# Optimization experiments

Measured on AMD Instinct MI355X. Metric: run time of the kernel, lower is better.

The kernel has to match this reference:

```python
import jax, jax.numpy as jnp
import numpy as np

B, T, C, H = 4, 4096, 1024, 128

def setup_inputs() -> dict:
    key = jax.random.key(0)
    kx, kk, kq, kv = jax.random.split(key, 4)
    scale = 1.0 / np.sqrt(C)  # mimic Linear init scale
    return {
        'x':  jax.random.normal(kx, (B, T, C), dtype=jnp.float32),
        'Wk': jax.random.normal(kk, (C, H), dtype=jnp.float32) * scale,
        'Wq': jax.random.normal(kq, (C, H), dtype=jnp.float32) * scale,
        'Wv': jax.random.normal(kv, (C, H), dtype=jnp.float32) * scale,
    }

def reference(x, Wk, Wq, Wv):
    # x: [B,T,C]; projections to [B,T,H]
    k = jnp.einsum('btc,ch->bth', x, Wk)
    q = jnp.einsum('btc,ch->bth', x, Wq)
    v = jnp.einsum('btc,ch->bth', x, Wv)
    scale = jnp.asarray(x.shape[-1] and (k.shape[-1] ** -0.5), dtype=x.dtype)
    # scores: [B,T,T]
    scores = jnp.einsum('bqh,bkh->bqk', q, k) * scale
    Tn = x.shape[1]
    causal = jnp.tril(jnp.ones((Tn, Tn), dtype=bool))
    scores = jnp.where(causal[None, :, :], scores, -jnp.inf)
    attn = jax.nn.softmax(scores, axis=-1)
    # dropout=0.0 -> identity
    out = jnp.einsum('bqk,bkh->bqh', attn, v)
    return out
```

## Files before the change

### kernel.cpp

```cpp
#include <hip/hip_runtime.h>
#include <hip/hip_bf16.h>
#include <math.h>

#define B_ 4
#define T_ 4096
#define C_ 1024
#define H_ 128
#define SCALE 0.08838834764831845f

typedef __attribute__((ext_vector_type(8))) short bf16x8;
typedef __attribute__((ext_vector_type(4))) float f32x4;

__device__ __forceinline__ unsigned short f2bf(float f) {
    union { float f; unsigned u; } x; x.f = f;
    unsigned r = x.u + 0x7FFF + ((x.u >> 16) & 1);
    return (unsigned short)(r >> 16);
}
__device__ __forceinline__ float bf2f(unsigned short u) {
    union { unsigned u; float f; } x; x.u = ((unsigned)u) << 16;
    return x.f;
}
__device__ __forceinline__ unsigned cvt_pk_bf16(float a, float b) {
    unsigned r;
    asm("v_cvt_pk_bf16_f32 %0, %1, %2" : "=v"(r) : "v"(a), "v"(b));
    return r;
}

#define GLOAD16(gsrc, ldst)                                                        \
    __builtin_amdgcn_global_load_lds(                                              \
        (const __attribute__((address_space(1))) unsigned int*)(gsrc),             \
        (__attribute__((address_space(3))) unsigned int*)(ldst), 16, 0, 0)

__global__ __launch_bounds__(256) void wtrans_kernel(
        const float* __restrict__ Wk, const float* __restrict__ Wq,
        const float* __restrict__ Wv, unsigned short* __restrict__ Wt) {
    int tid = blockIdx.x * 256 + threadIdx.x;
    int t = tid >> 17;
    int r = tid & 131071;
    int c = r >> 7;
    int h = r & 127;
    const float* W = (t == 0) ? Wk : (t == 1) ? Wq : Wv;
    Wt[t * 131072 + h * 1024 + c] = f2bf(W[r]);
}

__global__ __launch_bounds__(256) void qkv_gemm(
        const float* __restrict__ x, const unsigned short* __restrict__ Wt,
        unsigned short* __restrict__ qkv) {
    __shared__ unsigned short As[64][72];
    __shared__ unsigned short Bs[384][72];

    const int m0 = blockIdx.x * 64;
    const int tid = threadIdx.x;
    const int lane = tid & 63;
    const int w = tid >> 6;
    const int fr = lane & 15;
    const int fq = lane >> 4;

    f32x4 acc[6][4];
#pragma unroll
    for (int i = 0; i < 6; i++)
#pragma unroll
        for (int rf = 0; rf < 4; rf++) acc[i][rf] = f32x4{0.f, 0.f, 0.f, 0.f};

    for (int k0 = 0; k0 < C_; k0 += 64) {
        __syncthreads();
        {
            int row = tid >> 2;
            int coff = (tid & 3) * 16;
            const float* src = x + (long)(m0 + row) * C_ + k0 + coff;
            unsigned short tmp[16];
#pragma unroll
            for (int i = 0; i < 4; i++) {
                float4 v = ((const float4*)src)[i];
                tmp[i*4+0] = f2bf(v.x); tmp[i*4+1] = f2bf(v.y);
                tmp[i*4+2] = f2bf(v.z); tmp[i*4+3] = f2bf(v.w);
            }
            uint4* dst = (uint4*)&As[row][coff];
            dst[0] = ((uint4*)tmp)[0];
            dst[1] = ((uint4*)tmp)[1];
        }
#pragma unroll
        for (int i = 0; i < 12; i++) {
            int idx = tid + i * 256;
            int row = idx >> 3;
            int coff = (idx & 7) * 8;
            *(uint4*)&Bs[row][coff] =
                *(const uint4*)(Wt + (long)row * 1024 + k0 + coff);
        }
        __syncthreads();

#pragma unroll
        for (int kk = 0; kk < 2; kk++) {
            bf16x8 a[4], bb[6];
#pragma unroll
            for (int rf = 0; rf < 4; rf++)
                a[rf] = *(const bf16x8*)&As[rf*16 + fr][kk*32 + fq*8];
#pragma unroll
            for (int i = 0; i < 6; i++)
                bb[i] = *(const bf16x8*)&Bs[(w*6 + i)*16 + fr][kk*32 + fq*8];
#pragma unroll
            for (int i = 0; i < 6; i++)
#pragma unroll
                for (int rf = 0; rf < 4; rf++)
                    acc[i][rf] = __builtin_amdgcn_mfma_f32_16x16x32_bf16(
                        a[rf], bb[i], acc[i][rf], 0, 0, 0);
        }
    }
#pragma unroll
    for (int i = 0; i < 6; i++) {
        int nf = w*6 + i;
        int t = nf >> 3;
        int col = (nf & 7) * 16 + fr;
#pragma unroll
        for (int rf = 0; rf < 4; rf++)
#pragma unroll
            for (int r = 0; r < 4; r++) {
                int row = m0 + rf*16 + fq*4 + r;
                qkv[(long)t * (16384L * 128) + (long)row * 128 + col] = f2bf(acc[i][rf][r]);
            }
    }
}

__global__ __launch_bounds__(256) void vtrans_kernel(
        const unsigned short* __restrict__ v, unsigned short* __restrict__ vT) {
    __shared__ unsigned short tile[64][136];
    const int t0 = (blockIdx.x & 63) * 64;
    const int b = blockIdx.x >> 6;
    const int tid = threadIdx.x;
#pragma unroll
    for (int i = 0; i < 4; i++) {
        int idx = tid + i * 256;
        int tr = idx >> 4, coff = (idx & 15) * 8;
        *(uint4*)&tile[tr][coff] =
            *(const uint4*)(v + ((long)(b * T_ + t0 + tr)) * H_ + coff);
    }
    __syncthreads();
#pragma unroll
    for (int i = 0; i < 4; i++) {
        int idx = tid + i * 256;
        int h = idx >> 3, ts = (idx & 7) * 8;
        unsigned short tmp[8];
#pragma unroll
        for (int j = 0; j < 8; j++) tmp[j] = tile[ts + j][h];
        *(uint4*)(vT + ((long)(b * H_ + h)) * T_ + t0 + ts) = *(uint4*)tmp;
    }
}

__global__ __launch_bounds__(512, 4) void flash6_kernel(
        const unsigned short* __restrict__ qkv,
        const unsigned short* __restrict__ vT,
        unsigned short* __restrict__ po0, unsigned short* __restrict__ po1,
        unsigned short* __restrict__ po2, unsigned short* __restrict__ po3,
        float* __restrict__ pm, float* __restrict__ pl) {
    __shared__ unsigned short k_lds[2][64][128];
    __shared__ unsigned short v_lds[2][128][64];

    const int n = blockIdx.x;
    const int half = n >> 8;
    const int m = n & 255;
    const int b = (m & 7) >> 1;
    const int r = ((m >> 3) << 1) | (m & 1);
    const int jj = r & 31;
    const int pq = r >> 5;
    const int qt = half ? (31 - jj) : jj;
    const int p = half * 2 + pq;
    const int q0 = qt * 128;
    const int ntt = (qt + 1) * 2;
    const int t0 = (p * ntt) >> 2;
    const int t1 = ((p + 1) * ntt) >> 2;

    const int tid = threadIdx.x;
    const int w = tid >> 6;
    const int lane = tid & 63;
    const int fr = lane & 15;
    const int fq = lane >> 4;

    const unsigned short* kbase = qkv + (long)b * T_ * H_;
    const unsigned short* vbase = vT + (long)b * H_ * T_;

    const int kcolb0 = ((lane & 15) << 4) ^ ((((lane >> 4)) & 7) << 4);
    const int kcolb1 = ((lane & 15) << 4) ^ (((4 + (lane >> 4)) & 7) << 4);
    const int krl = lane >> 4;
    const int vrl = lane >> 3;
    const int vcolb = ((lane & 7) << 4) ^ (vrl << 4);
    unsigned short* const klds_flat = &k_lds[0][0][0];
    unsigned short* const vlds_flat = &v_lds[0][0][0];

    const int scol = ((fq ^ (fr & 7)) << 4);

    bf16x8 qf[4];
    {
        const unsigned short* qptr = qkv + 2097152 + ((long)b*T_ + q0 + w*16 + fr) * H_;
#pragma unroll
        for (int ks = 0; ks < 4; ks++)
            qf[ks] = *(const bf16x8*)(qptr + ks*32 + fq*8);
    }

    f32x4 acc[8];
#pragma unroll
    for (int i = 0; i < 8; i++) acc[i] = f32x4{0.f, 0.f, 0.f, 0.f};
    float m_r = -INFINITY, l_r = 0.f;
    const int qrow = q0 + w*16 + fr;

    int cur = 0;
    if (t0 < t1) {
        const int kv0 = t0 * 64;
#pragma unroll
        for (int i = 0; i < 2; i++) {
            int kcolb = i ? kcolb1 : kcolb0;
            GLOAD16(kbase + (long)(kv0 + 8*w + 4*i + krl) * 128 + (kcolb >> 1),
                    klds_flat + w*1024 + i*512);
            GLOAD16(vbase + (long)(16*w + 8*i + vrl) * 4096 + kv0 + (vcolb >> 1),
                    vlds_flat + w*1024 + i*512);
        }
    }

    for (int t = t0; t < t1; ++t) {
        const int kv0 = t * 64;
        __syncthreads();
        if (t + 1 < t1) {
            const int kv0n = kv0 + 64;
            const int boff = (cur ^ 1) * 8192;
#pragma unroll
            for (int i = 0; i < 2; i++) {
                int kcolb = i ? kcolb1 : kcolb0;
                GLOAD16(kbase + (long)(kv0n + 8*w + 4*i + krl) * 128 + (kcolb >> 1),
                        klds_flat + boff + w*1024 + i*512);
                GLOAD16(vbase + (long)(16*w + 8*i + vrl) * 4096 + kv0n + (vcolb >> 1),
                        vlds_flat + boff + w*1024 + i*512);
            }
            asm volatile("s_waitcnt vmcnt(4)" ::: "memory");
        } else {
            asm volatile("s_waitcnt vmcnt(0)" ::: "memory");
        }
        __syncthreads();

        const char* kl = (const char*)k_lds + cur*16384 + fr*256;
        const char* vl = (const char*)v_lds + cur*16384 + fr*128;

        f32x4 s[4];
#pragma unroll
        for (int sf = 0; sf < 4; sf++) s[sf] = f32x4{0.f,0.f,0.f,0.f};
        __builtin_amdgcn_s_setprio(1);
#pragma unroll
        for (int sf = 0; sf < 4; sf++)
#pragma unroll
            for (int ks = 0; ks < 4; ks++) {
                bf16x8 kf = *(const bf16x8*)(kl + sf*4096 + (scol ^ (ks << 6)));
                s[sf] = __builtin_amdgcn_mfma_f32_16x16x32_bf16(kf, qf[ks], s[sf], 0, 0, 0);
            }
        __builtin_amdgcn_s_setprio(0);

        float mx = -INFINITY;
        if (kv0 + 63 > q0 + 16*w) {
#pragma unroll
            for (int sf = 0; sf < 4; sf++)
#pragma unroll
                for (int rr = 0; rr < 4; rr++) {
                    int kv = kv0 + sf*16 + fq*4 + rr;
                    float sv = s[sf][rr] * SCALE;
                    sv = (kv > qrow) ? -INFINITY : sv;
                    s[sf][rr] = sv;
                    mx = fmaxf(mx, sv);
                }
        } else {
#pragma unroll
            for (int sf = 0; sf < 4; sf++)
#pragma unroll
                for (int rr = 0; rr < 4; rr++) {
                    float sv = s[sf][rr] * SCALE;
                    s[sf][rr] = sv;
                    mx = fmaxf(mx, sv);
                }
        }
        mx = fmaxf(mx, __shfl_xor(mx, 16, 64));
        mx = fmaxf(mx, __shfl_xor(mx, 32, 64));

        const bool skip = __all((m_r > -1e37f) & (mx - m_r <= 8.f));
        float msub;
        if (skip) {
            msub = m_r;
        } else {
            float mn = fmaxf(m_r, mx);
            msub = (mn == -INFINITY) ? 0.f : mn;
            float alpha = __expf(m_r - msub);
            m_r = mn;
#pragma unroll
            for (int hf = 0; hf < 8; hf++)
#pragma unroll
                for (int rr = 0; rr < 4; rr++) acc[hf][rr] *= alpha;
            l_r *= alpha;
        }

        float pv[4][4];
        float sum = 0.f;
#pragma unroll
        for (int sf = 0; sf < 4; sf++)
#pragma unroll
            for (int rr = 0; rr < 4; rr++) {
                float e = __expf(s[sf][rr] - msub);
                pv[sf][rr] = e;
                sum += e;
            }
        sum += __shfl_xor(sum, 16, 64);
        sum += __shfl_xor(sum, 32, 64);
        l_r += sum;

        unsigned pw[8];
#pragma unroll
        for (int sf = 0; sf < 4; sf++) {
            pw[2*sf]   = cvt_pk_bf16(pv[sf][0], pv[sf][1]);
            pw[2*sf+1] = cvt_pk_bf16(pv[sf][2], pv[sf][3]);
        }
        unsigned pbu[2][4];
        pbu[0][0]=0;pbu[0][1]=0;pbu[0][2]=0;pbu[0][3]=0;
        pbu[1][0]=0;pbu[1][1]=0;pbu[1][2]=0;pbu[1][3]=0;
        const int L1 = fr + 16 * ((fq & 1) * 2);
        const int L2 = L1 + 16;
        const int sel = (fq >> 1) & 1;
#pragma unroll
        for (int sf = 0; sf < 4; sf++) {
            unsigned w0 = (unsigned)__shfl((int)pw[2*sf],   L1, 64);
            unsigned w1 = (unsigned)__shfl((int)pw[2*sf+1], L1, 64);
            unsigned w2 = (unsigned)__shfl((int)pw[2*sf],   L2, 64);
            unsigned w3 = (unsigned)__shfl((int)pw[2*sf+1], L2, 64);
            if ((sf & 1) == sel) {
                int k2 = sf >> 1;
                pbu[k2][0] = w0; pbu[k2][1] = w1; pbu[k2][2] = w2; pbu[k2][3] = w3;
            }
        }
        union { unsigned u[4]; bf16x8 v; } pb0c, pb1c;
#pragma unroll
        for (int i = 0; i < 4; i++) { pb0c.u[i] = pbu[0][i]; pb1c.u[i] = pbu[1][i]; }
        bf16x8 pb0 = pb0c.v, pb1 = pb1c.v;

        __builtin_amdgcn_s_setprio(1);
#pragma unroll
        for (int hf = 0; hf < 8; hf++) {
            bf16x8 vf0 = *(const bf16x8*)(vl + hf*2048 + scol);
            bf16x8 vf1 = *(const bf16x8*)(vl + hf*2048 + (scol ^ 64));
            acc[hf] = __builtin_amdgcn_mfma_f32_16x16x32_bf16(vf0, pb0, acc[hf], 0, 0, 0);
            acc[hf] = __builtin_amdgcn_mfma_f32_16x16x32_bf16(vf1, pb1, acc[hf], 0, 0, 0);
        }
        __builtin_amdgcn_s_setprio(0);
        cur ^= 1;
    }

    unsigned short* po = (p == 0) ? po0 : (p == 1) ? po1 : (p == 2) ? po2 : po3;
    float linv = (l_r > 0.f) ? (1.0f / l_r) : 0.f;
    const long obase = ((long)b * T_ + qrow) * H_;
#pragma unroll
    for (int hf = 0; hf < 8; hf++) {
        unsigned u0 = cvt_pk_bf16(acc[hf][0] * linv, acc[hf][1] * linv);
        unsigned u1 = cvt_pk_bf16(acc[hf][2] * linv, acc[hf][3] * linv);
        uint2 uu; uu.x = u0; uu.y = u1;
        *(uint2*)(po + obase + hf*16 + fq*4) = uu;
    }
    if (fq == 0) {
        pm[p * 16384 + b * T_ + qrow] = m_r;
        pl[p * 16384 + b * T_ + qrow] = l_r;
    }
}

__global__ __launch_bounds__(256) void combine_kernel(
        const unsigned short* __restrict__ po0,
        const unsigned short* __restrict__ po1,
        const unsigned short* __restrict__ po2,
        const unsigned short* __restrict__ po3,
        const float* __restrict__ pm, const float* __restrict__ pl,
        float* __restrict__ out) {
    int idx = blockIdx.x * 256 + threadIdx.x;
    int row = idx >> 4;
    int seg = idx & 15;
    float mv[4], lv[4];
#pragma unroll
    for (int i = 0; i < 4; i++) { mv[i] = pm[i*16384 + row]; lv[i] = pl[i*16384 + row]; }
    float m = fmaxf(fmaxf(mv[0], mv[1]), fmaxf(mv[2], mv[3]));
    float wv[4]; float tot = 0.f;
#pragma unroll
    for (int i = 0; i < 4; i++) {
        wv[i] = (lv[i] > 0.f) ? __expf(mv[i] - m) * lv[i] : 0.f;
        tot += wv[i];
    }
    float inv = 1.0f / tot;
    long off = (long)row * H_ + seg * 8;
    unsigned short ua[8], ub[8], uc[8], ud[8];
    *(uint4*)ua = *(const uint4*)(po0 + off);
    *(uint4*)ub = *(const uint4*)(po1 + off);
    *(uint4*)uc = *(const uint4*)(po2 + off);
    *(uint4*)ud = *(const uint4*)(po3 + off);
    float* o = out + off;
#pragma unroll
    for (int j2 = 0; j2 < 8; j2++)
        o[j2] = inv * (wv[0] * bf2f(ua[j2]) + wv[1] * bf2f(ub[j2]) +
                       wv[2] * bf2f(uc[j2]) + wv[3] * bf2f(ud[j2]));
}

extern "C" void kernel_launch(void* const* d_in, const int* in_sizes, int n_in,
                              void* d_out, int out_size, void* d_ws, size_t ws_size,
                              hipStream_t stream) {
    (void)in_sizes; (void)n_in; (void)out_size; (void)ws_size;
    const float* x  = (const float*)d_in[0];
    const float* Wk = (const float*)d_in[1];
    const float* Wq = (const float*)d_in[2];
    const float* Wv = (const float*)d_in[3];
    float* out = (float*)d_out;

    unsigned short* Wt  = (unsigned short*)d_ws;
    unsigned short* qkv = Wt + 393216;
    unsigned short* vT  = qkv + 6291456;
    unsigned short* po0 = vT + 2097152;
    unsigned short* po1 = po0 + 2097152;
    unsigned short* po3 = po1 + 2097152;
    unsigned short* po2 = qkv + 4194304;
    float* pm = (float*)d_ws;
    float* pl = pm + 65536;

    wtrans_kernel<<<1536, 256, 0, stream>>>(Wk, Wq, Wv, Wt);
    qkv_gemm<<<256, 256, 0, stream>>>(x, Wt, qkv);
    vtrans_kernel<<<256, 256, 0, stream>>>(qkv + 4194304, vT);
    flash6_kernel<<<512, 512, 0, stream>>>(qkv, vT, po0, po1, po2, po3, pm, pl);
    combine_kernel<<<1024, 256, 0, stream>>>(po0, po1, po2, po3, pm, pl, out);
}
```

Before: 96.51 us.

## Double-buffer QKV GEMM, split N across blocks, fuse V transpose into epilogue

The QKV projection GEMM now splits the 384 output columns into two halves, so twice as many blocks run with fewer accumulators each. It double-buffers the x and W tiles, using global_load_lds async copies with swizzled LDS for W and register prefetch for x, and remaps block order for locality. The V output is written directly in transposed layout from the GEMM epilogue, which removes the separate vtrans kernel launch and its round trip through memory. In exchange, each x tile is loaded and converted twice, once per column half, and the transposed V writes are narrower and strided.

```diff
diff --git a/kernel.cpp b/kernel.cpp
--- a/kernel.cpp
+++ b/kernel.cpp
@@ -24,6 +24,14 @@
     unsigned r;
     asm("v_cvt_pk_bf16_f32 %0, %1, %2" : "=v"(r) : "v"(a), "v"(b));
     return r;
+}
+__device__ __forceinline__ void cvt16(const float4& a, const float4& b,
+                                      const float4& c, const float4& d,
+                                      unsigned short* t) {
+    t[0]=f2bf(a.x);  t[1]=f2bf(a.y);  t[2]=f2bf(a.z);  t[3]=f2bf(a.w);
+    t[4]=f2bf(b.x);  t[5]=f2bf(b.y);  t[6]=f2bf(b.z);  t[7]=f2bf(b.w);
+    t[8]=f2bf(c.x);  t[9]=f2bf(c.y);  t[10]=f2bf(c.z); t[11]=f2bf(c.w);
+    t[12]=f2bf(d.x); t[13]=f2bf(d.y); t[14]=f2bf(d.z); t[15]=f2bf(d.w);
 }
 
 #define GLOAD16(gsrc, ldst)                                                        \
@@ -43,106 +51,124 @@
     Wt[t * 131072 + h * 1024 + c] = f2bf(W[r]);
 }
 
-__global__ __launch_bounds__(256) void qkv_gemm(
+__global__ __launch_bounds__(256, 2) void qkv_gemm2(
         const float* __restrict__ x, const unsigned short* __restrict__ Wt,
-        unsigned short* __restrict__ qkv) {
-    __shared__ unsigned short As[64][72];
-    __shared__ unsigned short Bs[384][72];
-
-    const int m0 = blockIdx.x * 64;
+        unsigned short* __restrict__ qkv, unsigned short* __restrict__ vT) {
+    __shared__ unsigned short As[2][64][72];
+    __shared__ unsigned short Bs[2][192][64];
+
+    const int nsw = blockIdx.x;
+    const int sw = (nsw & 7) * 64 + (nsw >> 3);
+    const int m0 = (sw >> 1) * 64;
+    const int nh = sw & 1;
+
     const int tid = threadIdx.x;
     const int lane = tid & 63;
     const int w = tid >> 6;
     const int fr = lane & 15;
     const int fq = lane >> 4;
 
-    f32x4 acc[6][4];
+    const int xrow = tid >> 2, xco = (tid & 3) * 16;
+    const float* xsrc = x + (long)(m0 + xrow) * C_ + xco;
+    const int brl = lane >> 3;
+    const int bcolb = (((lane & 7) ^ brl) << 4);
+    unsigned short* const bs_flat = &Bs[0][0][0];
+    const unsigned short* wbase = Wt + (long)(nh * 192) * 1024;
+
+    f32x4 acc[3][4];
+#pragma unroll
+    for (int i = 0; i < 3; i++)
+#pragma unroll
+        for (int rf = 0; rf < 4; rf++) acc[i][rf] = f32x4{0.f, 0.f, 0.f, 0.f};
+
+    float4 xr0, xr1, xr2, xr3;
+    xr0 = ((const float4*)xsrc)[0]; xr1 = ((const float4*)xsrc)[1];
+    xr2 = ((const float4*)xsrc)[2]; xr3 = ((const float4*)xsrc)[3];
 #pragma unroll
     for (int i = 0; i < 6; i++)
-#pragma unroll
-        for (int rf = 0; rf < 4; rf++) acc[i][rf] = f32x4{0.f, 0.f, 0.f, 0.f};
-
-    for (int k0 = 0; k0 < C_; k0 += 64) {
+        GLOAD16(wbase + (long)(48*w + 8*i + brl) * 1024 + (bcolb >> 1),
+                bs_flat + (w*6 + i) * 512);
+    {
+        unsigned short tmp[16];
+        cvt16(xr0, xr1, xr2, xr3, tmp);
+        *(uint4*)&As[0][xrow][xco]     = ((uint4*)tmp)[0];
+        *(uint4*)&As[0][xrow][xco + 8] = ((uint4*)tmp)[1];
+    }
+
+    int cur = 0;
+    for (int k = 0; k < 16; ++k) {
         __syncthreads();
-        {
-            int row = tid >> 2;
-            int coff = (tid & 3) * 16;
-            const float* src = x + (long)(m0 + row) * C_ + k0 + coff;
-            unsigned short tmp[16];
-#pragma unroll
-            for (int i = 0; i < 4; i++) {
-                float4 v = ((const float4*)src)[i];
-                tmp[i*4+0] = f2bf(v.x); tmp[i*4+1] = f2bf(v.y);
-                tmp[i*4+2] = f2bf(v.z); tmp[i*4+3] = f2bf(v.w);
-            }
-            uint4* dst = (uint4*)&As[row][coff];
-            dst[0] = ((uint4*)tmp)[0];
-            dst[1] = ((uint4*)tmp)[1];
-        }
-#pragma unroll
-        for (int i = 0; i < 12; i++) {
-            int idx = tid + i * 256;
-            int row = idx >> 3;
-            int coff = (idx & 7) * 8;
-            *(uint4*)&Bs[row][coff] =
-                *(const uint4*)(Wt + (long)row * 1024 + k0 + coff);
+        const bool more = (k + 1) < 16;
+        if (more) {
+            const float* xs = xsrc + (k + 1) * 64;
+            xr0 = ((const float4*)xs)[0]; xr1 = ((const float4*)xs)[1];
+            xr2 = ((const float4*)xs)[2]; xr3 = ((const float4*)xs)[3];
+            const int boff = (cur ^ 1) * 12288;
+#pragma unroll
+            for (int i = 0; i < 6; i++)
+                GLOAD16(wbase + (long)(48*w + 8*i + brl) * 1024 + (k + 1) * 64 + (bcolb >> 1),
+                        bs_flat + boff + (w*6 + i) * 512);
+            asm volatile("s_waitcnt vmcnt(10)" ::: "memory");
+        } else {
+            asm volatile("s_waitcnt vmcnt(0)" ::: "memory");
         }
         __syncthreads();
 
+        const char* bsb = (const char*)bs_flat + cur * 24576;
+        __builtin_amdgcn_s_setprio(1);
 #pragma unroll
         for (int kk = 0; kk < 2; kk++) {
-            bf16x8 a[4], bb[6];
+            bf16x8 a[4], bb[3];
 #pragma unroll
             for (int rf = 0; rf < 4; rf++)
-                a[rf] = *(const bf16x8*)&As[rf*16 + fr][kk*32 + fq*8];
-#pragma unroll
-            for (int i = 0; i < 6; i++)
-                bb[i] = *(const bf16x8*)&Bs[(w*6 + i)*16 + fr][kk*32 + fq*8];
-#pragma unroll
-            for (int i = 0; i < 6; i++)
+                a[rf] = *(const bf16x8*)&As[cur][rf*16 + fr][kk*32 + fq*8];
+#pragma unroll
+            for (int i = 0; i < 3; i++) {
+                int row = (w*3 + i) * 16 + fr;
+                bb[i] = *(const bf16x8*)(bsb + row*128 + ((((kk<<2) + fq) ^ (fr & 7)) << 4));
+            }
+#pragma unroll
+            for (int i = 0; i < 3; i++)
 #pragma unroll
                 for (int rf = 0; rf < 4; rf++)
                     acc[i][rf] = __builtin_amdgcn_mfma_f32_16x16x32_bf16(
                         a[rf], bb[i], acc[i][rf], 0, 0, 0);
         }
-    }
-#pragma unroll
-    for (int i = 0; i < 6; i++) {
-        int nf = w*6 + i;
-        int t = nf >> 3;
-        int col = (nf & 7) * 16 + fr;
-#pragma unroll
-        for (int rf = 0; rf < 4; rf++)
-#pragma unroll
-            for (int r = 0; r < 4; r++) {
-                int row = m0 + rf*16 + fq*4 + r;
-                qkv[(long)t * (16384L * 128) + (long)row * 128 + col] = f2bf(acc[i][rf][r]);
-            }
-    }
-}
-
-__global__ __launch_bounds__(256) void vtrans_kernel(
-        const unsigned short* __restrict__ v, unsigned short* __restrict__ vT) {
-    __shared__ unsigned short tile[64][136];
-    const int t0 = (blockIdx.x & 63) * 64;
-    const int b = blockIdx.x >> 6;
-    const int tid = threadIdx.x;
-#pragma unroll
-    for (int i = 0; i < 4; i++) {
-        int idx = tid + i * 256;
-        int tr = idx >> 4, coff = (idx & 15) * 8;
-        *(uint4*)&tile[tr][coff] =
-            *(const uint4*)(v + ((long)(b * T_ + t0 + tr)) * H_ + coff);
-    }
-    __syncthreads();
-#pragma unroll
-    for (int i = 0; i < 4; i++) {
-        int idx = tid + i * 256;
-        int h = idx >> 3, ts = (idx & 7) * 8;
-        unsigned short tmp[8];
-#pragma unroll
-        for (int j = 0; j < 8; j++) tmp[j] = tile[ts + j][h];
-        *(uint4*)(vT + ((long)(b * H_ + h)) * T_ + t0 + ts) = *(uint4*)tmp;
+        __builtin_amdgcn_s_setprio(0);
+
+        if (more) {
+            unsigned short tmp[16];
+            cvt16(xr0, xr1, xr2, xr3, tmp);
+            *(uint4*)&As[cur ^ 1][xrow][xco]     = ((uint4*)tmp)[0];
+            *(uint4*)&As[cur ^ 1][xrow][xco + 8] = ((uint4*)tmp)[1];
+        }
+        cur ^= 1;
+    }
+
+#pragma unroll
+    for (int i = 0; i < 3; i++) {
+        int nfg = nh*12 + w*3 + i;
+        int t = nfg >> 3;
+        int col = (nfg & 7) * 16 + fr;
+        if (t < 2) {
+#pragma unroll
+            for (int rf = 0; rf < 4; rf++)
+#pragma unroll
+                for (int r = 0; r < 4; r++) {
+                    int row = m0 + rf*16 + fq*4 + r;
+                    qkv[(long)t * 2097152 + (long)row * 128 + col] = f2bf(acc[i][rf][r]);
+                }
+        } else {
+            const int bb_ = m0 >> 12;
+            const int trow = m0 & 4095;
+#pragma unroll
+            for (int rf = 0; rf < 4; rf++) {
+                uint2 uu;
+                uu.x = cvt_pk_bf16(acc[i][rf][0], acc[i][rf][1]);
+                uu.y = cvt_pk_bf16(acc[i][rf][2], acc[i][rf][3]);
+                *(uint2*)(vT + ((long)(bb_*128 + col)) * 4096 + trow + rf*16 + fq*4) = uu;
+            }
+        }
     }
 }
 
@@ -185,7 +211,6 @@
     const int vcolb = ((lane & 7) << 4) ^ (vrl << 4);
     unsigned short* const klds_flat = &k_lds[0][0][0];
     unsigned short* const vlds_flat = &v_lds[0][0][0];
-
     const int scol = ((fq ^ (fr & 7)) << 4);
 
     bf16x8 qf[4];
@@ -351,9 +376,9 @@
     const long obase = ((long)b * T_ + qrow) * H_;
 #pragma unroll
     for (int hf = 0; hf < 8; hf++) {
-        unsigned u0 = cvt_pk_bf16(acc[hf][0] * linv, acc[hf][1] * linv);
-        unsigned u1 = cvt_pk_bf16(acc[hf][2] * linv, acc[hf][3] * linv);
-        uint2 uu; uu.x = u0; uu.y = u1;
+        uint2 uu;
+        uu.x = cvt_pk_bf16(acc[hf][0] * linv, acc[hf][1] * linv);
+        uu.y = cvt_pk_bf16(acc[hf][2] * linv, acc[hf][3] * linv);
         *(uint2*)(po + obase + hf*16 + fq*4) = uu;
     }
     if (fq == 0) {
@@ -362,7 +387,7 @@
     }
 }
 
-__global__ __launch_bounds__(256) void combine_kernel(
+__global__ __launch_bounds__(256) void combine4_kernel(
         const unsigned short* __restrict__ po0,
         const unsigned short* __restrict__ po1,
         const unsigned short* __restrict__ po2,
@@ -417,8 +442,7 @@
     float* pl = pm + 65536;
 
     wtrans_kernel<<<1536, 256, 0, stream>>>(Wk, Wq, Wv, Wt);
-    qkv_gemm<<<256, 256, 0, stream>>>(x, Wt, qkv);
-    vtrans_kernel<<<256, 256, 0, stream>>>(qkv + 4194304, vT);
+    qkv_gemm2<<<512, 256, 0, stream>>>(x, Wt, qkv, vT);
     flash6_kernel<<<512, 512, 0, stream>>>(qkv, vT, po0, po1, po2, po3, pm, pl);
-    combine_kernel<<<1024, 256, 0, stream>>>(po0, po1, po2, po3, pm, pl, out);
-}
+    combine4_kernel<<<1024, 256, 0, stream>>>(po0, po1, po2, po3, pm, pl, out);
+}
```

Result: faster. 83.30 us (-13.7%).
